# Kernel tuning notes

Measured on AMD Instinct MI355X. Metric: run time of the kernel, lower is better.

Reference implementation:

```python
import jax, jax.numpy as jnp
import numpy as np

B, L, H, NH = 4, 512, 512, 8
DK = H // NH
REPR_IN, REPR_HID = 53, 32
NEG_INF = -jnp.inf


def _mask_by_1dmask(x, mask):
    # x: [B, NH, L, L], mask: [B, L] bool
    m2 = mask[:, :, None] & mask[:, None, :]              # [B, L, L]
    xm = jnp.where(m2[:, None, :, :], x, NEG_INF)
    all_inf = jnp.all(xm == NEG_INF, axis=-1, keepdims=True)
    return jnp.where(all_inf, 0.0, xm)


def _layernorm(x, g, b, eps=1e-5):
    mu = jnp.mean(x, axis=-1, keepdims=True)
    var = jnp.var(x, axis=-1, keepdims=True)
    return (x - mu) * jax.lax.rsqrt(var + eps) * g + b


def setup_inputs() -> dict:
    key = jax.random.key(0)
    ks = jax.random.split(key, 16)
    s = 1.0 / np.sqrt(H)
    inp = {
        "x": jax.random.normal(ks[0], (B, L, H), jnp.float32),
        "mask": jax.random.randint(ks[1], (B, L), 0, 2).astype(bool),
        "refCov": jax.random.normal(ks[2], (B, L, L, REPR_IN), jnp.float32),
        "wq": jax.random.normal(ks[3], (H, H), jnp.float32) * s,
        "bq": jnp.zeros((H,), jnp.float32),
        "wk": jax.random.normal(ks[4], (H, H), jnp.float32) * s,
        "bk": jnp.zeros((H,), jnp.float32),
        "wv": jax.random.normal(ks[5], (H, H), jnp.float32) * s,
        "bv": jnp.zeros((H,), jnp.float32),
        "wo": jax.random.normal(ks[6], (H, H), jnp.float32) * s,
        "bo": jnp.zeros((H,), jnp.float32),
        "r1w": jax.random.normal(ks[7], (REPR_IN, REPR_HID), jnp.float32) / np.sqrt(REPR_IN),
        "r1b": jnp.zeros((REPR_HID,), jnp.float32),
        "r2w": jax.random.normal(ks[8], (REPR_HID, NH), jnp.float32) / np.sqrt(REPR_HID),
        "r2b": jnp.zeros((NH,), jnp.float32),
        "ln_g": jnp.ones((H,), jnp.float32),
        "ln_b": jnp.zeros((H,), jnp.float32),
    }
    return inp


def reference(x, mask, refCov, wq, bq, wk, bk, wv, bv, wo, bo, r1w, r1b, r2w, r2b, ln_g, ln_b):
    Bc, Lc, Hc = x.shape
    residual = x
    q = (x @ wq + bq).reshape(Bc, Lc, NH, DK).transpose(0, 2, 1, 3)  # [B,NH,L,DK]
    k = (x @ wk + bk).reshape(Bc, Lc, NH, DK).transpose(0, 2, 1, 3)
    v = (x @ wv + bv).reshape(Bc, Lc, NH, DK).transpose(0, 2, 1, 3)

    scores = jnp.einsum("bhid,bhjd->bhij", q, k) / np.sqrt(DK)
    scores = _mask_by_1dmask(scores, mask)
    attn = jax.nn.softmax(scores, axis=-1)

    # ref-covariate attention weights via small MLP: [B,L,L,53] -> [B,L,L,NH]
    ref = jax.nn.relu(refCov @ r1w + r1b) @ r2w + r2b
    ref = ref.transpose(0, 3, 1, 2)                        # [B,NH,L,L]
    ref = _mask_by_1dmask(ref, mask)
    ref = jax.nn.softmax(ref, axis=-1)

    comb = attn + ref
    comb = comb / jnp.sum(comb, axis=-1, keepdims=True)

    out = jnp.einsum("bhij,bhjd->bhid", comb, v)           # [B,NH,L,DK]
    out = out.transpose(0, 2, 1, 3).reshape(Bc, Lc, Hc)
    out = out @ wo + bo
    return _layernorm(residual + out, ln_g, ln_b)
```

## Files before the change

kernel.cpp:

```cpp
#include <hip/hip_runtime.h>
#include <math.h>

#define BB 4
#define LL 512
#define HH 512
#define NHH 8
#define DKK 64
#define RIN 53

__global__ __launch_bounds__(256) void k_qkv(
    const float* __restrict__ x,
    const float* __restrict__ wq, const float* __restrict__ bq,
    const float* __restrict__ wk, const float* __restrict__ bk,
    const float* __restrict__ wv, const float* __restrict__ bv,
    float* __restrict__ qb, float* __restrict__ kb, float* __restrict__ vb)
{
    __shared__ float As[64][20];
    __shared__ float Bs[16][64];

    const int t  = threadIdx.x;
    const int bm = blockIdx.x;
    const int bn = blockIdx.y;
    const int mat = bn >> 3;
    const float* w    = (mat == 0) ? wq : (mat == 1) ? wk : wv;
    const float* bias = (mat == 0) ? bq : (mat == 1) ? bk : bv;
    float* dst        = (mat == 0) ? qb : (mat == 1) ? kb : vb;
    const int n0 = (bn & 7) * 64;

    const int tx = t & 15, ty = t >> 4;
    float acc[4][4] = {};

    const int ar = t >> 2, ak4 = t & 3;
    const int wkk = t >> 4, wn4 = t & 15;

    for (int k0 = 0; k0 < HH; k0 += 16) {
        *(float4*)(&As[ar][ak4 * 4]) =
            *(const float4*)(x + (bm * 64 + ar) * HH + k0 + ak4 * 4);
        *(float4*)(&Bs[wkk][wn4 * 4]) =
            *(const float4*)(w + (k0 + wkk) * HH + n0 + wn4 * 4);
        __syncthreads();
#pragma unroll
        for (int kk = 0; kk < 16; ++kk) {
            const float a0 = As[ty * 4 + 0][kk];
            const float a1 = As[ty * 4 + 1][kk];
            const float a2 = As[ty * 4 + 2][kk];
            const float a3 = As[ty * 4 + 3][kk];
            const float4 b4 = *(const float4*)(&Bs[kk][tx * 4]);
            acc[0][0] = fmaf(a0, b4.x, acc[0][0]); acc[0][1] = fmaf(a0, b4.y, acc[0][1]);
            acc[0][2] = fmaf(a0, b4.z, acc[0][2]); acc[0][3] = fmaf(a0, b4.w, acc[0][3]);
            acc[1][0] = fmaf(a1, b4.x, acc[1][0]); acc[1][1] = fmaf(a1, b4.y, acc[1][1]);
            acc[1][2] = fmaf(a1, b4.z, acc[1][2]); acc[1][3] = fmaf(a1, b4.w, acc[1][3]);
            acc[2][0] = fmaf(a2, b4.x, acc[2][0]); acc[2][1] = fmaf(a2, b4.y, acc[2][1]);
            acc[2][2] = fmaf(a2, b4.z, acc[2][2]); acc[2][3] = fmaf(a2, b4.w, acc[2][3]);
            acc[3][0] = fmaf(a3, b4.x, acc[3][0]); acc[3][1] = fmaf(a3, b4.y, acc[3][1]);
            acc[3][2] = fmaf(a3, b4.z, acc[3][2]); acc[3][3] = fmaf(a3, b4.w, acc[3][3]);
        }
        __syncthreads();
    }

    const int ncol = n0 + tx * 4;
    const float4 b4 = *(const float4*)(bias + ncol);
    const int h = ncol >> 6, d0 = ncol & 63;
#pragma unroll
    for (int i = 0; i < 4; ++i) {
        const int grow = bm * 64 + ty * 4 + i;
        const int b = grow >> 9, iseq = grow & 511;
        float4 r;
        r.x = acc[i][0] + b4.x; r.y = acc[i][1] + b4.y;
        r.z = acc[i][2] + b4.z; r.w = acc[i][3] + b4.w;
        *(float4*)(dst + ((size_t)(b * NHH + h) * LL + iseq) * DKK + d0) = r;
    }
}

__global__ __launch_bounds__(256) void k_refmlp(
    const float* __restrict__ refCov,
    const float* __restrict__ r1w, const float* __restrict__ r1b,
    const float* __restrict__ r2w, const float* __restrict__ r2b,
    float* __restrict__ ref)
{
    __shared__ float cov[256 * RIN];

    const int t = threadIdx.x;
    const size_t base = (size_t)blockIdx.x * (256 * RIN);

    {
        const float4* src = (const float4*)(refCov + base);
        float4* dst = (float4*)cov;
#pragma unroll
        for (int p = 0; p < 13; ++p) dst[p * 256 + t] = src[p * 256 + t];
        if (t < 64) dst[13 * 256 + t] = src[13 * 256 + t];
    }
    __syncthreads();

    const int pi = blockIdx.x * 256 + t;
    const int j  = pi & 511;
    const int bi = pi >> 9;
    const int b  = bi >> 9, i = bi & 511;
    const float* cw = cov + t * RIN;

    float hid[32];
#pragma unroll
    for (int h = 0; h < 32; ++h) hid[h] = r1b[h];

#pragma unroll 4
    for (int kk = 0; kk < RIN; ++kk) {
        const float c = cw[kk];
#pragma unroll
        for (int h = 0; h < 32; ++h)
            hid[h] = fmaf(c, r1w[kk * 32 + h], hid[h]);
    }

    float out[8];
#pragma unroll
    for (int o = 0; o < 8; ++o) out[o] = r2b[o];
#pragma unroll
    for (int h = 0; h < 32; ++h) {
        const float hv = fmaxf(hid[h], 0.0f);
#pragma unroll
        for (int o = 0; o < 8; ++o)
            out[o] = fmaf(hv, r2w[h * 8 + o], out[o]);
    }
#pragma unroll
    for (int o = 0; o < 8; ++o)
        ref[((size_t)(b * NHH + o) * LL + i) * LL + j] = out[o];
}

__global__ __launch_bounds__(256, 2) void k_attn_comb(
    const float* __restrict__ qb, const float* __restrict__ kb,
    const int* __restrict__ mask,
    float* refcomb)
{
    __shared__ float4 q4s[16][32];
    __shared__ float4 k4s[16][128];
    __shared__ float  mval[LL];

    const int t  = threadIdx.x;
    const int bh = blockIdx.x;
    const int b  = bh >> 3;
    const int i0 = blockIdx.y * 32;
    const int r  = t >> 3, c = t & 7;

    {
        const int d4 = t >> 4, r0 = t & 15;
#pragma unroll
        for (int p = 0; p < 2; ++p) {
            const int rr = r0 + p * 16;
            q4s[d4][rr] = *(const float4*)(qb + ((size_t)bh * LL + i0 + rr) * DKK + d4 * 4);
        }
#pragma unroll
        for (int p = 0; p < 2; ++p) {
            const int jj = t + p * 256;
            mval[jj] = (mask[b * LL + jj] != 0) ? 1.0f : 0.0f;
        }
    }

    float s0[16], s1[16], s2[16], s3[16];
    float rv0[16], rv1[16], rv2[16], rv3[16];

    auto compChunk = [&](float (&SS)[16], int CH) {
        {
            const int d4s = t >> 4, jb0 = t & 15;
#pragma unroll
            for (int p = 0; p < 8; ++p) {
                const int jl = jb0 + p * 16;
                k4s[d4s][jl] =
                    *(const float4*)(kb + ((size_t)bh * LL + CH * 128 + jl) * DKK + d4s * 4);
            }
        }
        __syncthreads();
#pragma unroll
        for (int mm = 0; mm < 16; ++mm) SS[mm] = 0.0f;
        for (int d4 = 0; d4 < 16; ++d4) {
            const float4 qv = q4s[d4][r];
#pragma unroll
            for (int mm = 0; mm < 16; ++mm) {
                const float4 kv = k4s[d4][c + 8 * mm];
                SS[mm] = fmaf(qv.x, kv.x, SS[mm]);
                SS[mm] = fmaf(qv.y, kv.y, SS[mm]);
                SS[mm] = fmaf(qv.z, kv.z, SS[mm]);
                SS[mm] = fmaf(qv.w, kv.w, SS[mm]);
            }
        }
        __syncthreads();
    };

    compChunk(s0, 0); compChunk(s1, 1); compChunk(s2, 2); compChunk(s3, 3);

    const bool rowv = mval[i0 + r] > 0.5f;
    float mx;
    bool  uni;
    float dsum;

    auto maskScale = [&](float (&SS)[16], int CH, float scale) {
#pragma unroll
        for (int mm = 0; mm < 16; ++mm) {
            const int jj = c + 8 * (CH * 16 + mm);
            const bool val = rowv && (mval[jj] > 0.5f);
            SS[mm] = val ? SS[mm] * scale : -INFINITY;
            mx = fmaxf(mx, SS[mm]);
        }
    };
    auto expSum = [&](float (&SS)[16]) {
#pragma unroll
        for (int mm = 0; mm < 16; ++mm) {
            float pv;
            if (uni)                       pv = 1.0f;
            else if (SS[mm] == -INFINITY)  pv = 0.0f;
            else                           pv = __expf(SS[mm] - mx);
            SS[mm] = pv; dsum += pv;
        }
    };
    auto red8max = [&](float v) {
        for (int o = 1; o < 8; o <<= 1) v = fmaxf(v, __shfl_xor(v, o, 64));
        return v;
    };
    auto red8sum = [&](float v) {
        for (int o = 1; o < 8; o <<= 1) v += __shfl_xor(v, o, 64);
        return v;
    };

    mx = -INFINITY;
    maskScale(s0, 0, 0.125f); maskScale(s1, 1, 0.125f);
    maskScale(s2, 2, 0.125f); maskScale(s3, 3, 0.125f);
    mx = red8max(mx);
    uni = (mx == -INFINITY);
    dsum = 0.0f;
    expSum(s0); expSum(s1); expSum(s2); expSum(s3);
    const float da = red8sum(dsum);

    {
        const float* rrow = refcomb + ((size_t)bh * LL + i0 + r) * LL;
#pragma unroll
        for (int mm = 0; mm < 16; ++mm) {
            rv0[mm] = rrow[c + 8 * mm];
            rv1[mm] = rrow[c + 8 * (16 + mm)];
            rv2[mm] = rrow[c + 8 * (32 + mm)];
            rv3[mm] = rrow[c + 8 * (48 + mm)];
        }
    }
    mx = -INFINITY;
    maskScale(rv0, 0, 1.0f); maskScale(rv1, 1, 1.0f);
    maskScale(rv2, 2, 1.0f); maskScale(rv3, 3, 1.0f);
    mx = red8max(mx);
    uni = (mx == -INFINITY);
    dsum = 0.0f;
    expSum(rv0); expSum(rv1); expSum(rv2); expSum(rv3);
    const float dr = red8sum(dsum);

    const float invda = 1.0f / da, invdr = 1.0f / dr;
    float tsum = 0.0f;
    auto combSum = [&](float (&SS)[16], float (&TT)[16]) {
#pragma unroll
        for (int mm = 0; mm < 16; ++mm) {
            const float cm = SS[mm] * invda + TT[mm] * invdr;
            SS[mm] = cm; tsum += cm;
        }
    };
    combSum(s0, rv0); combSum(s1, rv1); combSum(s2, rv2); combSum(s3, rv3);
    const float invt = 1.0f / red8sum(tsum);

    {
        float* orow = refcomb + ((size_t)bh * LL + i0 + r) * LL;
#pragma unroll
        for (int mm = 0; mm < 16; ++mm) {
            orow[c + 8 * mm]        = s0[mm] * invt;
            orow[c + 8 * (16 + mm)] = s1[mm] * invt;
            orow[c + 8 * (32 + mm)] = s2[mm] * invt;
            orow[c + 8 * (48 + mm)] = s3[mm] * invt;
        }
    }
}

__device__ inline void fma4(float4& a, float s, const float4& b) {
    a.x = fmaf(s, b.x, a.x); a.y = fmaf(s, b.y, a.y);
    a.z = fmaf(s, b.z, a.z); a.w = fmaf(s, b.w, a.w);
}

__global__ __launch_bounds__(256) void k_pv(
    const float* __restrict__ comb, const float* __restrict__ vb,
    float* __restrict__ aout)
{
    __shared__ float cs[64][68];
    __shared__ float vs[64][64];

    const int t  = threadIdx.x;
    const int bh = blockIdx.x, b = bh >> 3, h = bh & 7;
    const int i0 = blockIdx.y * 64;
    const int dq = t & 15, rg = t >> 4;
    float4 acc[4] = {};

    for (int k0 = 0; k0 < LL; k0 += 64) {
#pragma unroll
        for (int p = 0; p < 4; ++p) {
            const int flat = p * 256 + t;
            const int row = flat >> 4, k4 = flat & 15;
            *(float4*)(&cs[row][k4 * 4]) =
                *(const float4*)(comb + ((size_t)bh * LL + i0 + row) * LL + k0 + k4 * 4);
            *(float4*)(&vs[row][k4 * 4]) =
                *(const float4*)(vb + ((size_t)bh * LL + k0 + row) * DKK + k4 * 4);
        }
        __syncthreads();
#pragma unroll
        for (int kk4 = 0; kk4 < 16; ++kk4) {
            float4 vv[4];
#pragma unroll
            for (int q = 0; q < 4; ++q)
                vv[q] = *(const float4*)(&vs[kk4 * 4 + q][dq * 4]);
#pragma unroll
            for (int rr = 0; rr < 4; ++rr) {
                const float4 cv = *(const float4*)(&cs[rg * 4 + rr][kk4 * 4]);
                fma4(acc[rr], cv.x, vv[0]);
                fma4(acc[rr], cv.y, vv[1]);
                fma4(acc[rr], cv.z, vv[2]);
                fma4(acc[rr], cv.w, vv[3]);
            }
        }
        __syncthreads();
    }
#pragma unroll
    for (int rr = 0; rr < 4; ++rr) {
        const int i = i0 + rg * 4 + rr;
        *(float4*)(aout + ((size_t)(b * LL + i) * NHH + h) * DKK + dq * 4) = acc[rr];
    }
}

__global__ __launch_bounds__(256) void k_proj_ln(
    const float* __restrict__ aout, const float* __restrict__ wo,
    const float* __restrict__ bo, const float* __restrict__ x,
    const float* __restrict__ ln_g, const float* __restrict__ ln_b,
    float* __restrict__ out)
{
    __shared__ float xs[8][20];
    __shared__ float ws[16][512];

    const int t   = threadIdx.x;
    const int m0  = blockIdx.x * 8;
    const int row = t >> 5;
    const int c16 = t & 31;
    float4 acc[4] = {};

    for (int k0 = 0; k0 < HH; k0 += 16) {
        if (t < 32) {
            const int rr = t >> 2, k4 = t & 3;
            *(float4*)(&xs[rr][k4 * 4]) =
                *(const float4*)(aout + (size_t)(m0 + rr) * HH + k0 + k4 * 4);
        }
#pragma unroll
        for (int p = 0; p < 8; ++p) {
            const int flat = p * 256 + t;
            const int kk = flat >> 7, n4 = flat & 127;
            *(float4*)(&ws[kk][n4 * 4]) =
                *(const float4*)(wo + (size_t)(k0 + kk) * HH + n4 * 4);
        }
        __syncthreads();
#pragma unroll
        for (int kk = 0; kk < 16; ++kk) {
            const float xv = xs[row][kk];
#pragma unroll
            for (int q = 0; q < 4; ++q) {
                const float4 wv = *(const float4*)(&ws[kk][c16 * 4 + q * 128]);
                fma4(acc[q], xv, wv);
            }
        }
        __syncthreads();
    }

    const int grow = m0 + row;
    float4 v4[4];
    float sum = 0.0f, sq = 0.0f;
#pragma unroll
    for (int q = 0; q < 4; ++q) {
        const int col = c16 * 4 + q * 128;
        const float4 b4 = *(const float4*)(bo + col);
        const float4 r4 = *(const float4*)(x + (size_t)grow * HH + col);
        float4 tv;
        tv.x = acc[q].x + b4.x + r4.x;
        tv.y = acc[q].y + b4.y + r4.y;
        tv.z = acc[q].z + b4.z + r4.z;
        tv.w = acc[q].w + b4.w + r4.w;
        v4[q] = tv;
        sum += tv.x + tv.y + tv.z + tv.w;
        sq  += tv.x * tv.x + tv.y * tv.y + tv.z * tv.z + tv.w * tv.w;
    }
#pragma unroll
    for (int o = 1; o < 32; o <<= 1) {
        sum += __shfl_xor(sum, o, 64);
        sq  += __shfl_xor(sq, o, 64);
    }
    const float mu  = sum * (1.0f / 512.0f);
    const float var = sq * (1.0f / 512.0f) - mu * mu;
    const float rs  = rsqrtf(var + 1e-5f);
#pragma unroll
    for (int q = 0; q < 4; ++q) {
        const int col = c16 * 4 + q * 128;
        const float4 g4 = *(const float4*)(ln_g + col);
        const float4 be4 = *(const float4*)(ln_b + col);
        float4 o4;
        o4.x = (v4[q].x - mu) * rs * g4.x + be4.x;
        o4.y = (v4[q].y - mu) * rs * g4.y + be4.y;
        o4.z = (v4[q].z - mu) * rs * g4.z + be4.z;
        o4.w = (v4[q].w - mu) * rs * g4.w + be4.w;
        *(float4*)(out + (size_t)grow * HH + col) = o4;
    }
}

extern "C" void kernel_launch(void* const* d_in, const int* in_sizes, int n_in,
                              void* d_out, int out_size, void* d_ws, size_t ws_size,
                              hipStream_t stream)
{
    const float* x      = (const float*)d_in[0];
    const int*   mask   = (const int*)d_in[1];
    const float* refCov = (const float*)d_in[2];
    const float* wq = (const float*)d_in[3];
    const float* bq = (const float*)d_in[4];
    const float* wk = (const float*)d_in[5];
    const float* bk = (const float*)d_in[6];
    const float* wv = (const float*)d_in[7];
    const float* bv = (const float*)d_in[8];
    const float* wo = (const float*)d_in[9];
    const float* bo = (const float*)d_in[10];
    const float* r1w = (const float*)d_in[11];
    const float* r1b = (const float*)d_in[12];
    const float* r2w = (const float*)d_in[13];
    const float* r2b = (const float*)d_in[14];
    const float* ln_g = (const float*)d_in[15];
    const float* ln_b = (const float*)d_in[16];
    float* out = (float*)d_out;

    float* ws   = (float*)d_ws;
    float* qb   = ws;
    float* kb   = qb + 1048576;
    float* vb   = kb + 1048576;
    float* refc = vb + 1048576;
    float* aout = refc + 8388608;

    k_qkv     <<<dim3(32, 24), 256, 0, stream>>>(x, wq, bq, wk, bk, wv, bv, qb, kb, vb);
    k_refmlp  <<<4096,         256, 0, stream>>>(refCov, r1w, r1b, r2w, r2b, refc);
    k_attn_comb<<<dim3(32, 16), 256, 0, stream>>>(qb, kb, mask, refc);
    k_pv      <<<dim3(32, 8),  256, 0, stream>>>(refc, vb, aout);
    k_proj_ln <<<256,          256, 0, stream>>>(aout, wo, bo, x, ln_g, ln_b, out);
}
```

Baseline: 545.4 us.

## Fuse P·V into attention-combine kernel, dropping combined-probability round trip

The attention/ref softmax combine kernel now multiplies the combined probabilities by V directly from registers, staging V chunks in shared memory and reducing partial sums across the 8 lanes of each row with shuffles. This removes writing the full B×NH×L×L combined matrix back to global memory and the separate PV kernel that reread it. In exchange the fused kernel holds 16 float4 accumulators per thread, which raises register pressure, and it adds extra barriers and shuffle reductions.

```diff
diff --git a/kernel.cpp b/kernel.cpp
--- a/kernel.cpp
+++ b/kernel.cpp
@@ -7,6 +7,18 @@
 #define NHH 8
 #define DKK 64
 #define RIN 53
+
+__device__ inline void fma4(float4& a, float s, const float4& b) {
+    a.x = fmaf(s, b.x, a.x); a.y = fmaf(s, b.y, a.y);
+    a.z = fmaf(s, b.z, a.z); a.w = fmaf(s, b.w, a.w);
+}
+__device__ inline float4 add4(const float4& a, const float4& b) {
+    return make_float4(a.x + b.x, a.y + b.y, a.z + b.z, a.w + b.w);
+}
+__device__ inline float4 shfl_xor4(const float4& v, int m) {
+    return make_float4(__shfl_xor(v.x, m, 64), __shfl_xor(v.y, m, 64),
+                       __shfl_xor(v.z, m, 64), __shfl_xor(v.w, m, 64));
+}
 
 __global__ __launch_bounds__(256) void k_qkv(
     const float* __restrict__ x,
@@ -125,10 +137,11 @@
         ref[((size_t)(b * NHH + o) * LL + i) * LL + j] = out[o];
 }
 
-__global__ __launch_bounds__(256, 2) void k_attn_comb(
+__global__ __launch_bounds__(256, 2) void k_attn_pv(
     const float* __restrict__ qb, const float* __restrict__ kb,
-    const int* __restrict__ mask,
-    float* refcomb)
+    const float* __restrict__ vb, const int* __restrict__ mask,
+    const float* __restrict__ refc,
+    float* __restrict__ aout)
 {
     __shared__ float4 q4s[16][32];
     __shared__ float4 k4s[16][128];
@@ -136,7 +149,7 @@
 
     const int t  = threadIdx.x;
     const int bh = blockIdx.x;
-    const int b  = bh >> 3;
+    const int b  = bh >> 3, h = bh & 7;
     const int i0 = blockIdx.y * 32;
     const int r  = t >> 3, c = t & 7;
 
@@ -229,7 +242,7 @@
     const float da = red8sum(dsum);
 
     {
-        const float* rrow = refcomb + ((size_t)bh * LL + i0 + r) * LL;
+        const float* rrow = refc + ((size_t)bh * LL + i0 + r) * LL;
 #pragma unroll
         for (int mm = 0; mm < 16; ++mm) {
             rv0[mm] = rrow[c + 8 * mm];
@@ -259,69 +272,64 @@
     combSum(s0, rv0); combSum(s1, rv1); combSum(s2, rv2); combSum(s3, rv3);
     const float invt = 1.0f / red8sum(tsum);
 
-    {
-        float* orow = refcomb + ((size_t)bh * LL + i0 + r) * LL;
+    float4 acc[16];
+#pragma unroll
+    for (int d4 = 0; d4 < 16; ++d4) acc[d4] = make_float4(0.f, 0.f, 0.f, 0.f);
+
+    auto pvChunk = [&](float (&SS)[16], int CH) {
+        __syncthreads();
+        {
+            const int d4s = t >> 4, jb0 = t & 15;
+#pragma unroll
+            for (int p = 0; p < 8; ++p) {
+                const int jl = jb0 + p * 16;
+                k4s[d4s][jl] =
+                    *(const float4*)(vb + ((size_t)bh * LL + CH * 128 + jl) * DKK + d4s * 4);
+            }
+        }
+        __syncthreads();
 #pragma unroll
         for (int mm = 0; mm < 16; ++mm) {
-            orow[c + 8 * mm]        = s0[mm] * invt;
-            orow[c + 8 * (16 + mm)] = s1[mm] * invt;
-            orow[c + 8 * (32 + mm)] = s2[mm] * invt;
-            orow[c + 8 * (48 + mm)] = s3[mm] * invt;
-        }
-    }
-}
-
-__device__ inline void fma4(float4& a, float s, const float4& b) {
-    a.x = fmaf(s, b.x, a.x); a.y = fmaf(s, b.y, a.y);
-    a.z = fmaf(s, b.z, a.z); a.w = fmaf(s, b.w, a.w);
-}
-
-__global__ __launch_bounds__(256) void k_pv(
-    const float* __restrict__ comb, const float* __restrict__ vb,
-    float* __restrict__ aout)
-{
-    __shared__ float cs[64][68];
-    __shared__ float vs[64][64];
-
-    const int t  = threadIdx.x;
-    const int bh = blockIdx.x, b = bh >> 3, h = bh & 7;
-    const int i0 = blockIdx.y * 64;
-    const int dq = t & 15, rg = t >> 4;
-    float4 acc[4] = {};
-
-    for (int k0 = 0; k0 < LL; k0 += 64) {
-#pragma unroll
-        for (int p = 0; p < 4; ++p) {
-            const int flat = p * 256 + t;
-            const int row = flat >> 4, k4 = flat & 15;
-            *(float4*)(&cs[row][k4 * 4]) =
-                *(const float4*)(comb + ((size_t)bh * LL + i0 + row) * LL + k0 + k4 * 4);
-            *(float4*)(&vs[row][k4 * 4]) =
-                *(const float4*)(vb + ((size_t)bh * LL + k0 + row) * DKK + k4 * 4);
-        }
-        __syncthreads();
-#pragma unroll
-        for (int kk4 = 0; kk4 < 16; ++kk4) {
-            float4 vv[4];
-#pragma unroll
-            for (int q = 0; q < 4; ++q)
-                vv[q] = *(const float4*)(&vs[kk4 * 4 + q][dq * 4]);
-#pragma unroll
-            for (int rr = 0; rr < 4; ++rr) {
-                const float4 cv = *(const float4*)(&cs[rg * 4 + rr][kk4 * 4]);
-                fma4(acc[rr], cv.x, vv[0]);
-                fma4(acc[rr], cv.y, vv[1]);
-                fma4(acc[rr], cv.z, vv[2]);
-                fma4(acc[rr], cv.w, vv[3]);
-            }
-        }
-        __syncthreads();
-    }
-#pragma unroll
-    for (int rr = 0; rr < 4; ++rr) {
-        const int i = i0 + rg * 4 + rr;
-        *(float4*)(aout + ((size_t)(b * LL + i) * NHH + h) * DKK + dq * 4) = acc[rr];
-    }
+            const float p = SS[mm];
+            const int jl = c + 8 * mm;
+#pragma unroll
+            for (int d4 = 0; d4 < 16; ++d4)
+                fma4(acc[d4], p, k4s[d4][jl]);
+        }
+    };
+    pvChunk(s0, 0); pvChunk(s1, 1); pvChunk(s2, 2); pvChunk(s3, 3);
+
+    const bool k4lo = (c & 4) == 0;
+    float4 r8[8];
+#pragma unroll
+    for (int i = 0; i < 8; ++i) {
+        const float4 keep = k4lo ? acc[i] : acc[i + 8];
+        const float4 send = k4lo ? acc[i + 8] : acc[i];
+        r8[i] = add4(keep, shfl_xor4(send, 4));
+    }
+    const bool k2lo = (c & 2) == 0;
+    float4 r4[4];
+#pragma unroll
+    for (int i = 0; i < 4; ++i) {
+        const float4 keep = k2lo ? r8[i] : r8[i + 4];
+        const float4 send = k2lo ? r8[i + 4] : r8[i];
+        r4[i] = add4(keep, shfl_xor4(send, 2));
+    }
+    const bool k1lo = (c & 1) == 0;
+    float4 r2[2];
+#pragma unroll
+    for (int i = 0; i < 2; ++i) {
+        const float4 keep = k1lo ? r4[i] : r4[i + 2];
+        const float4 send = k1lo ? r4[i + 2] : r4[i];
+        r2[i] = add4(keep, shfl_xor4(send, 1));
+    }
+#pragma unroll
+    for (int i = 0; i < 2; ++i) {
+        r2[i].x *= invt; r2[i].y *= invt; r2[i].z *= invt; r2[i].w *= invt;
+    }
+    float* dst = aout + ((size_t)((b * LL + i0 + r) * NHH + h)) * DKK + c * 8;
+    *(float4*)(dst)     = r2[0];
+    *(float4*)(dst + 4) = r2[1];
 }
 
 __global__ __launch_bounds__(256) void k_proj_ln(
@@ -436,7 +444,6 @@
 
     k_qkv     <<<dim3(32, 24), 256, 0, stream>>>(x, wq, bq, wk, bk, wv, bv, qb, kb, vb);
     k_refmlp  <<<4096,         256, 0, stream>>>(refCov, r1w, r1b, r2w, r2b, refc);
-    k_attn_comb<<<dim3(32, 16), 256, 0, stream>>>(qb, kb, mask, refc);
-    k_pv      <<<dim3(32, 8),  256, 0, stream>>>(refc, vb, aout);
+    k_attn_pv <<<dim3(32, 16), 256, 0, stream>>>(qb, kb, vb, mask, refc, aout);
     k_proj_ln <<<256,          256, 0, stream>>>(aout, wo, bo, x, ln_g, ln_b, out);
 }
```

Result: slower. 567.4 us (+4.0%).
